# Optimization experiments

Measured on AMD Instinct MI355X. Metric: run time of the kernel, lower is better.

Reference implementation:

```python
import jax, jax.numpy as jnp
import numpy as np

ATOM_FDIM = 39
BOND_FDIM = 11
MAX_NB = 6
N_ATOMS = 100_000
N_BONDS = 200_001  # index 0 is the padding bond
N_MOLS = 1000
HIDDEN = 256
DEPTH = 6


def setup_inputs() -> dict:
    key = jax.random.key(0)
    ks = jax.random.split(key, 8)
    fatoms = jax.random.normal(ks[0], (N_ATOMS, ATOM_FDIM), dtype=jnp.float32)
    fbonds = jax.random.normal(ks[1], (N_BONDS, ATOM_FDIM + BOND_FDIM), dtype=jnp.float32)
    fbonds = fbonds.at[0].set(0.0)  # padding bond has zero features, as in tensorize()
    agraph = jax.random.randint(ks[2], (N_ATOMS, MAX_NB), 0, N_BONDS, dtype=jnp.int64 if jax.config.jax_enable_x64 else jnp.int32)
    bgraph = jax.random.randint(ks[3], (N_BONDS, MAX_NB), 0, N_BONDS, dtype=agraph.dtype)
    bgraph = bgraph.at[0].set(0)
    mol_ids = jnp.sort(jax.random.randint(ks[4], (N_ATOMS,), 0, N_MOLS, dtype=agraph.dtype))
    scale_i = 1.0 / np.sqrt(ATOM_FDIM + BOND_FDIM)
    scale_h = 1.0 / np.sqrt(HIDDEN)
    scale_o = 1.0 / np.sqrt(ATOM_FDIM + HIDDEN)
    W_i = jax.random.normal(ks[5], (HIDDEN, ATOM_FDIM + BOND_FDIM), dtype=jnp.float32) * scale_i
    W_h = jax.random.normal(ks[6], (HIDDEN, HIDDEN), dtype=jnp.float32) * scale_h
    W_o = jax.random.normal(ks[7], (HIDDEN, ATOM_FDIM + HIDDEN), dtype=jnp.float32) * scale_o
    b_o = jnp.zeros((HIDDEN,), dtype=jnp.float32)
    return {
        'fatoms': fatoms, 'fbonds': fbonds, 'agraph': agraph, 'bgraph': bgraph,
        'mol_ids': mol_ids, 'n_mols': N_MOLS, 'depth': DEPTH,
        'W_i': W_i, 'W_h': W_h, 'W_o': W_o, 'b_o': b_o,
    }


def reference(fatoms, fbonds, agraph, bgraph, mol_ids, n_mols, depth, W_i, W_h, W_o, b_o):
    # binput: [E, H]; message passing over directed bond graph
    binput = fbonds @ W_i.T
    message = jax.nn.relu(binput)
    for _ in range(depth - 1):
        nei = message[bgraph].sum(axis=1)          # [E, MAX_NB, H] gather -> [E, H]
        message = jax.nn.relu(binput + nei @ W_h.T)
    nei = message[agraph].sum(axis=1)              # [N, H]
    ainput = jnp.concatenate([fatoms, nei], axis=1)
    atom_hiddens = jax.nn.relu(ainput @ W_o.T + b_o)  # [N, H]
    # per-molecule mean (equivalent to the scope-based slicing mean)
    sums = jax.ops.segment_sum(atom_hiddens, mol_ids, num_segments=n_mols)
    counts = jax.ops.segment_sum(jnp.ones((atom_hiddens.shape[0],), dtype=atom_hiddens.dtype), mol_ids, num_segments=n_mols)
    mol_vecs = sums / jnp.maximum(counts, 1.0)[:, None]
    return mol_vecs
```

## Files before the change

### kernel.cpp

```cpp
#include <hip/hip_runtime.h>

#define HID 256
#define AS_LD 72
#define TB_LD 264

typedef unsigned short u16;
typedef unsigned int u32;
typedef short bf16x8 __attribute__((ext_vector_type(8)));
typedef float f32x4 __attribute__((ext_vector_type(4)));
typedef u16 u16x8 __attribute__((ext_vector_type(8)));

static __device__ __forceinline__ float bf2f(u16 b) {
    u32 u = ((u32)b) << 16;
    return __uint_as_float(u);
}
static __device__ __forceinline__ u16 f2bf(float f) {
    u32 u = __float_as_uint(f);
    return (u16)((u + 0x7FFFu + ((u >> 16) & 1u)) >> 16);
}

__global__ __launch_bounds__(512, 4) void fused_layer(
    const u16* __restrict__ Sg, const int* __restrict__ graph, int c1,
    const u16* __restrict__ Bd, int ldbd, int c2,
    const float* __restrict__ Cf, int ldcf, int Kc, int c3,
    const u16* __restrict__ WB, int ldw,
    const float* __restrict__ bias,
    u16* __restrict__ C, int M)
{
    __shared__ __align__(16) u16 lds[2 * 64 * AS_LD];

    const int t    = threadIdx.x;
    const int w    = t >> 6;
    const int lane = t & 63;
    const int row0 = blockIdx.x * 64;
    const int wc   = w * 32;
    const int fr   = lane & 15;
    const int fq   = lane >> 4;

    const int g  = t & 7;
    const int ra = t >> 3;
    const int gr = row0 + ra;
    const int grc = gr < M ? gr : 0;

    int nbi[6];
    const u16* bdp = nullptr;
    if (c1 > 0) {
        const int* gp = graph + (size_t)grc * 6;
        #pragma unroll
        for (int j = 0; j < 6; ++j) nbi[j] = gp[j];
    }
    if (c2 > 0) bdp = Bd + (size_t)grc * ldbd;

    const int nch = c1 + c2 + c3;
    const int nbf = c1 + c2;

    u16x8 va[6];
    float fa[8];

    auto issue = [&](int kc) {
        if (kc < c1) {
            #pragma unroll
            for (int j = 0; j < 6; ++j)
                va[j] = *(const u16x8*)(Sg + (size_t)nbi[j] * 256 + kc * 64 + g * 8);
        } else if (kc < nbf) {
            va[0] = *(const u16x8*)(bdp + (kc - c1) * 64 + g * 8);
        } else {
            const int kb = (kc - nbf) * 64 + g * 8;
            #pragma unroll
            for (int i = 0; i < 8; ++i)
                fa[i] = (gr < M && kb + i < Kc) ? Cf[(size_t)gr * ldcf + kb + i] : 0.f;
        }
    };

    auto consume = [&](int kc, u16* Ab) {
        u16 o[8];
        if (kc < c1) {
            float sa[8] = {};
            #pragma unroll
            for (int j = 0; j < 6; ++j)
                #pragma unroll
                for (int e = 0; e < 8; ++e) sa[e] += bf2f(va[j][e]);
            #pragma unroll
            for (int e = 0; e < 8; ++e) o[e] = f2bf(sa[e]);
        } else if (kc < nbf) {
            *(u16x8*)o = va[0];
        } else {
            #pragma unroll
            for (int i = 0; i < 8; ++i) o[i] = f2bf(fa[i]);
        }
        *(uint4*)(Ab + ra * AS_LD + g * 8) = *(const uint4*)o;
    };

    f32x4 acc[4][2] = {};
    issue(0);
    #pragma unroll 1
    for (int kc = 0; kc < nch; ++kc) {
        u16* Ab = lds + (kc & 1) * (64 * AS_LD);

        bf16x8 bq[2][2];
        #pragma unroll
        for (int s = 0; s < 2; ++s)
            #pragma unroll
            for (int j = 0; j < 2; ++j) {
                const int col = wc + j * 16 + fr;
                bq[s][j] = *(const bf16x8*)(WB + (size_t)col * ldw + kc * 64 + s * 32 + fq * 8);
            }

        consume(kc, Ab);

        if (kc + 1 < nch) issue(kc + 1);

        asm volatile("s_waitcnt lgkmcnt(0)" ::: "memory");
        __builtin_amdgcn_s_barrier();
        asm volatile("" ::: "memory");

        #pragma unroll
        for (int s = 0; s < 2; ++s) {
            bf16x8 af[4];
            #pragma unroll
            for (int i = 0; i < 4; ++i)
                af[i] = *(const bf16x8*)(Ab + (i * 16 + fr) * AS_LD + s * 32 + fq * 8);
            #pragma unroll
            for (int j = 0; j < 2; ++j)
                #pragma unroll
                for (int i = 0; i < 4; ++i)
                    acc[i][j] = __builtin_amdgcn_mfma_f32_16x16x32_bf16(bq[s][j], af[i], acc[i][j], 0, 0, 0);
        }
    }

    u16* Tb = lds;
    #pragma unroll
    for (int s2 = 0; s2 < 2; ++s2) {
        __syncthreads();
        #pragma unroll
        for (int j = 0; j < 2; ++j) {
            const int gc = wc + j * 16 + fq * 4;
            float4 bv = make_float4(0.f, 0.f, 0.f, 0.f);
            if (bias) bv = *(const float4*)&bias[gc];
            #pragma unroll
            for (int ii = 0; ii < 2; ++ii) {
                const int i = s2 * 2 + ii;
                u16 o[4];
                o[0] = f2bf(fmaxf(acc[i][j][0] + bv.x, 0.f));
                o[1] = f2bf(fmaxf(acc[i][j][1] + bv.y, 0.f));
                o[2] = f2bf(fmaxf(acc[i][j][2] + bv.z, 0.f));
                o[3] = f2bf(fmaxf(acc[i][j][3] + bv.w, 0.f));
                *(uint2*)(Tb + (ii * 16 + fr) * TB_LD + gc) = *(const uint2*)o;
            }
        }
        __syncthreads();
        const int gsl = t & 31;
        const int rb  = t >> 5;
        #pragma unroll
        for (int it2 = 0; it2 < 2; ++it2) {
            const int rl = it2 * 16 + rb;
            const int grr = row0 + s2 * 32 + rl;
            if (grr < M) {
                const u16x8 v = *(const u16x8*)(Tb + rl * TB_LD + gsl * 8);
                *(u16x8*)(C + (size_t)grr * 256 + gsl * 8) = v;
            }
        }
    }
}

__global__ void build_wb(const float* __restrict__ src1, int lds1, int off1, int k1,
                         const float* __restrict__ src2, int lds2, int off2, int k2,
                         u16* __restrict__ dst, int ldd)
{
    const int n = blockIdx.x;
    for (int k = threadIdx.x; k < ldd; k += blockDim.x) {
        float v = 0.f;
        if (k < k1)           v = src1[(size_t)n * lds1 + off1 + k];
        else if (k < k1 + k2) v = src2[(size_t)n * lds2 + off2 + (k - k1)];
        dst[(size_t)n * ldd + k] = f2bf(v);
    }
}

__global__ void build_fb(const float* __restrict__ fb, u16* __restrict__ FB, int E)
{
    const int e = blockIdx.x * 4 + (threadIdx.x >> 6);
    if (e >= E) return;
    const int k = threadIdx.x & 63;
    FB[(size_t)e * 64 + k] = (k < 50) ? f2bf(fb[(size_t)e * 50 + k]) : (u16)0;
}

__global__ void segment_mean(const u16* __restrict__ atomh, const int* __restrict__ mol_ids,
                             float* __restrict__ out, int N)
{
    const int m = blockIdx.x;
    const int t = threadIdx.x;
    __shared__ int s_lo, s_hi;
    if (t == 0) {
        int lo = 0, hi = N;
        while (lo < hi) { int mid = (lo + hi) >> 1; if (mol_ids[mid] < m) lo = mid + 1; else hi = mid; }
        s_lo = lo;
        lo = s_lo; hi = N;
        while (lo < hi) { int mid = (lo + hi) >> 1; if (mol_ids[mid] < m + 1) lo = mid + 1; else hi = mid; }
        s_hi = lo;
    }
    __syncthreads();
    const int lo = s_lo, hi = s_hi;
    float sum = 0.f;
    for (int a = lo; a < hi; ++a) sum += bf2f(atomh[(size_t)a * HID + t]);
    const float cnt = (float)((hi - lo) > 1 ? (hi - lo) : 1);
    out[(size_t)m * HID + t] = sum / cnt;
}

extern "C" void kernel_launch(void* const* d_in, const int* in_sizes, int n_in,
                              void* d_out, int out_size, void* d_ws, size_t ws_size,
                              hipStream_t stream)
{
    const float* fatoms = (const float*)d_in[0];
    const float* fbonds = (const float*)d_in[1];
    const int*   agraph = (const int*)d_in[2];
    const int*   bgraph = (const int*)d_in[3];
    const int*   mol_ids = (const int*)d_in[4];
    const float* W_i = (const float*)d_in[7];
    const float* W_h = (const float*)d_in[8];
    const float* W_o = (const float*)d_in[9];
    const float* b_o = (const float*)d_in[10];

    const int N = in_sizes[0] / 39;
    const int E = in_sizes[1] / 50;
    const int N_MOLS = 1000;
    const int DEPTH = 6;

    const size_t EH = (size_t)E * HID;
    const size_t wbh_sz = (size_t)256 * 320;
    const size_t wbi_sz = (size_t)256 * 64;
    const size_t wbo_sz = (size_t)256 * 320;
    const size_t wsz = wbh_sz + wbi_sz + wbo_sz;
    const size_t fb_sz = (size_t)E * 64;

    const size_t need_nofb = (2 * EH + wsz) * sizeof(u16);
    const size_t need_fb   = (2 * EH + fb_sz + wsz) * sizeof(u16);
    if (ws_size < need_nofb) return;
    const bool use_fb = (ws_size >= need_fb);

    u16* buf0 = (u16*)d_ws;
    u16* buf1 = buf0 + EH;
    u16* FB   = use_fb ? (buf1 + EH) : nullptr;
    u16* wbh  = (use_fb ? FB + fb_sz : buf1 + EH);
    u16* wbi  = wbh + wbh_sz;
    u16* wbo  = wbi + wbi_sz;

    float* out = (float*)d_out;

    build_wb<<<dim3(256), dim3(64), 0, stream>>>(W_h, 256, 0, 256, W_i, 50, 0, 50, wbh, 320);
    build_wb<<<dim3(256), dim3(64), 0, stream>>>(W_i, 50, 0, 50, W_i, 50, 0, 0, wbi, 64);
    build_wb<<<dim3(256), dim3(64), 0, stream>>>(W_o, 295, 39, 256, W_o, 295, 0, 39, wbo, 320);
    if (use_fb)
        build_fb<<<dim3((E + 3) / 4), dim3(256), 0, stream>>>(fbonds, FB, E);

    const int gE = (E + 63) / 64;
    const int gN = (N + 63) / 64;

    if (use_fb)
        fused_layer<<<dim3(gE), dim3(512), 0, stream>>>(
            nullptr, nullptr, 0, FB, 64, 1, nullptr, 0, 0, 0, wbi, 64, nullptr, buf0, E);
    else
        fused_layer<<<dim3(gE), dim3(512), 0, stream>>>(
            nullptr, nullptr, 0, nullptr, 0, 0, fbonds, 50, 50, 1, wbi, 64, nullptr, buf0, E);

    u16* src = buf0;
    u16* dst = buf1;
    for (int it = 0; it < DEPTH - 1; ++it) {
        if (use_fb)
            fused_layer<<<dim3(gE), dim3(512), 0, stream>>>(
                src, bgraph, 4, FB, 64, 1, nullptr, 0, 0, 0, wbh, 320, nullptr, dst, E);
        else
            fused_layer<<<dim3(gE), dim3(512), 0, stream>>>(
                src, bgraph, 4, nullptr, 0, 0, fbonds, 50, 50, 1, wbh, 320, nullptr, dst, E);
        u16* tmp = src; src = dst; dst = tmp;
    }

    fused_layer<<<dim3(gN), dim3(512), 0, stream>>>(
        src, agraph, 4, nullptr, 0, 0, fatoms, 39, 39, 1, wbo, 320, b_o, dst, N);

    segment_mean<<<dim3(N_MOLS), dim3(256), 0, stream>>>(dst, mol_ids, out, N);
}
```

Measured before the change: 914.4 us.

## Store bond messages as uint8 with per-64-column float scales

Message buffers between layers are now written as unsigned 8-bit values with one float scale per 64-column chunk, computed from a wave-shuffle max in the epilogue. The gather stage dequantizes neighbor rows on load, halving the bytes fetched in the memory-bound neighbor-sum. This adds extra scale loads and quantization arithmetic, and loses accuracy relative to bf16 storage, which may break tolerance. The fallback path without the bond-feature buffer is removed and a separate atom-hidden buffer is allocated.

```diff
diff --git a/kernel.cpp b/kernel.cpp
--- a/kernel.cpp
+++ b/kernel.cpp
@@ -5,10 +5,12 @@
 #define TB_LD 264
 
 typedef unsigned short u16;
+typedef unsigned char u8;
 typedef unsigned int u32;
 typedef short bf16x8 __attribute__((ext_vector_type(8)));
 typedef float f32x4 __attribute__((ext_vector_type(4)));
 typedef u16 u16x8 __attribute__((ext_vector_type(8)));
+typedef u8 u8x8 __attribute__((ext_vector_type(8)));
 
 static __device__ __forceinline__ float bf2f(u16 b) {
     u32 u = ((u32)b) << 16;
@@ -20,12 +22,13 @@
 }
 
 __global__ __launch_bounds__(512, 4) void fused_layer(
-    const u16* __restrict__ Sg, const int* __restrict__ graph, int c1,
+    const u8* __restrict__ Sg, const float* __restrict__ Ssc,
+    const int* __restrict__ graph, int c1,
     const u16* __restrict__ Bd, int ldbd, int c2,
     const float* __restrict__ Cf, int ldcf, int Kc, int c3,
     const u16* __restrict__ WB, int ldw,
     const float* __restrict__ bias,
-    u16* __restrict__ C, int M)
+    void* __restrict__ Cout, float* __restrict__ Csc, int M)
 {
     __shared__ __align__(16) u16 lds[2 * 64 * AS_LD];
 
@@ -54,16 +57,21 @@
     const int nch = c1 + c2 + c3;
     const int nbf = c1 + c2;
 
-    u16x8 va[6];
+    u8x8  va[6];
+    float sv[6];
+    u16x8 vb;
     float fa[8];
 
     auto issue = [&](int kc) {
         if (kc < c1) {
             #pragma unroll
             for (int j = 0; j < 6; ++j)
-                va[j] = *(const u16x8*)(Sg + (size_t)nbi[j] * 256 + kc * 64 + g * 8);
+                va[j] = *(const u8x8*)(Sg + (size_t)nbi[j] * 256 + kc * 64 + g * 8);
+            #pragma unroll
+            for (int j = 0; j < 6; ++j)
+                sv[j] = Ssc[(size_t)nbi[j] * 4 + kc];
         } else if (kc < nbf) {
-            va[0] = *(const u16x8*)(bdp + (kc - c1) * 64 + g * 8);
+            vb = *(const u16x8*)(bdp + (kc - c1) * 64 + g * 8);
         } else {
             const int kb = (kc - nbf) * 64 + g * 8;
             #pragma unroll
@@ -79,11 +87,11 @@
             #pragma unroll
             for (int j = 0; j < 6; ++j)
                 #pragma unroll
-                for (int e = 0; e < 8; ++e) sa[e] += bf2f(va[j][e]);
+                for (int e = 0; e < 8; ++e) sa[e] += (float)va[j][e] * sv[j];
             #pragma unroll
             for (int e = 0; e < 8; ++e) o[e] = f2bf(sa[e]);
         } else if (kc < nbf) {
-            *(u16x8*)o = va[0];
+            *(u16x8*)o = vb;
         } else {
             #pragma unroll
             for (int i = 0; i < 8; ++i) o[i] = f2bf(fa[i]);
@@ -129,6 +137,7 @@
     }
 
     u16* Tb = lds;
+    const bool quant = (Csc != nullptr);
     #pragma unroll
     for (int s2 = 0; s2 < 2; ++s2) {
         __syncthreads();
@@ -155,9 +164,27 @@
         for (int it2 = 0; it2 < 2; ++it2) {
             const int rl = it2 * 16 + rb;
             const int grr = row0 + s2 * 32 + rl;
-            if (grr < M) {
-                const u16x8 v = *(const u16x8*)(Tb + rl * TB_LD + gsl * 8);
-                *(u16x8*)(C + (size_t)grr * 256 + gsl * 8) = v;
+            const u16x8 v = *(const u16x8*)(Tb + rl * TB_LD + gsl * 8);
+            if (quant) {
+                float f[8];
+                float mx = 0.f;
+                #pragma unroll
+                for (int e = 0; e < 8; ++e) { f[e] = bf2f(v[e]); mx = fmaxf(mx, f[e]); }
+                mx = fmaxf(mx, __shfl_xor(mx, 1));
+                mx = fmaxf(mx, __shfl_xor(mx, 2));
+                mx = fmaxf(mx, __shfl_xor(mx, 4));
+                const float r = mx > 0.f ? 255.f / mx : 0.f;
+                u8x8 q;
+                #pragma unroll
+                for (int e = 0; e < 8; ++e) q[e] = (u8)(f[e] * r + 0.5f);
+                if (grr < M) {
+                    *(u8x8*)((u8*)Cout + (size_t)grr * 256 + gsl * 8) = q;
+                    if ((gsl & 7) == 0)
+                        Csc[(size_t)grr * 4 + (gsl >> 3)] = mx * (1.f / 255.f);
+                }
+            } else {
+                if (grr < M)
+                    *(u16x8*)((u16*)Cout + (size_t)grr * 256 + gsl * 8) = v;
             }
         }
     }
@@ -225,57 +252,54 @@
     const int N_MOLS = 1000;
     const int DEPTH = 6;
 
-    const size_t EH = (size_t)E * HID;
-    const size_t wbh_sz = (size_t)256 * 320;
-    const size_t wbi_sz = (size_t)256 * 64;
-    const size_t wbo_sz = (size_t)256 * 320;
-    const size_t wsz = wbh_sz + wbi_sz + wbo_sz;
-    const size_t fb_sz = (size_t)E * 64;
-
-    const size_t need_nofb = (2 * EH + wsz) * sizeof(u16);
-    const size_t need_fb   = (2 * EH + fb_sz + wsz) * sizeof(u16);
-    if (ws_size < need_nofb) return;
-    const bool use_fb = (ws_size >= need_fb);
-
-    u16* buf0 = (u16*)d_ws;
-    u16* buf1 = buf0 + EH;
-    u16* FB   = use_fb ? (buf1 + EH) : nullptr;
-    u16* wbh  = (use_fb ? FB + fb_sz : buf1 + EH);
-    u16* wbi  = wbh + wbh_sz;
-    u16* wbo  = wbi + wbi_sz;
+    const size_t q_sz  = (size_t)E * 256;
+    const size_t sc_sz = (size_t)E * 4 * 4;
+    const size_t fb_sz = (size_t)E * 64 * 2;
+    const size_t ah_sz = (size_t)N * HID * 2;
+    const size_t wbh_sz = (size_t)256 * 320 * 2;
+    const size_t wbi_sz = (size_t)256 * 64 * 2;
+    const size_t wbo_sz = (size_t)256 * 320 * 2;
+    const size_t need = 2 * q_sz + 2 * sc_sz + fb_sz + ah_sz + wbh_sz + wbi_sz + wbo_sz;
+    if (ws_size < need) return;
+
+    u8* p = (u8*)d_ws;
+    u8*    q0  = p;             p += q_sz;
+    u8*    q1  = p;             p += q_sz;
+    float* sc0 = (float*)p;     p += sc_sz;
+    float* sc1 = (float*)p;     p += sc_sz;
+    u16*   FB  = (u16*)p;       p += fb_sz;
+    u16*   ah  = (u16*)p;       p += ah_sz;
+    u16*   wbh = (u16*)p;       p += wbh_sz;
+    u16*   wbi = (u16*)p;       p += wbi_sz;
+    u16*   wbo = (u16*)p;
 
     float* out = (float*)d_out;
 
     build_wb<<<dim3(256), dim3(64), 0, stream>>>(W_h, 256, 0, 256, W_i, 50, 0, 50, wbh, 320);
     build_wb<<<dim3(256), dim3(64), 0, stream>>>(W_i, 50, 0, 50, W_i, 50, 0, 0, wbi, 64);
     build_wb<<<dim3(256), dim3(64), 0, stream>>>(W_o, 295, 39, 256, W_o, 295, 0, 39, wbo, 320);
-    if (use_fb)
-        build_fb<<<dim3((E + 3) / 4), dim3(256), 0, stream>>>(fbonds, FB, E);
+    build_fb<<<dim3((E + 3) / 4), dim3(256), 0, stream>>>(fbonds, FB, E);
 
     const int gE = (E + 63) / 64;
     const int gN = (N + 63) / 64;
 
-    if (use_fb)
+    fused_layer<<<dim3(gE), dim3(512), 0, stream>>>(
+        nullptr, nullptr, nullptr, 0, FB, 64, 1, nullptr, 0, 0, 0,
+        wbi, 64, nullptr, q0, sc0, E);
+
+    u8* src = q0;  float* ssc = sc0;
+    u8* dst = q1;  float* dsc = sc1;
+    for (int it = 0; it < DEPTH - 1; ++it) {
         fused_layer<<<dim3(gE), dim3(512), 0, stream>>>(
-            nullptr, nullptr, 0, FB, 64, 1, nullptr, 0, 0, 0, wbi, 64, nullptr, buf0, E);
-    else
-        fused_layer<<<dim3(gE), dim3(512), 0, stream>>>(
-            nullptr, nullptr, 0, nullptr, 0, 0, fbonds, 50, 50, 1, wbi, 64, nullptr, buf0, E);
-
-    u16* src = buf0;
-    u16* dst = buf1;
-    for (int it = 0; it < DEPTH - 1; ++it) {
-        if (use_fb)
-            fused_layer<<<dim3(gE), dim3(512), 0, stream>>>(
-                src, bgraph, 4, FB, 64, 1, nullptr, 0, 0, 0, wbh, 320, nullptr, dst, E);
-        else
-            fused_layer<<<dim3(gE), dim3(512), 0, stream>>>(
-                src, bgraph, 4, nullptr, 0, 0, fbonds, 50, 50, 1, wbh, 320, nullptr, dst, E);
-        u16* tmp = src; src = dst; dst = tmp;
+            src, ssc, bgraph, 4, FB, 64, 1, nullptr, 0, 0, 0,
+            wbh, 320, nullptr, dst, dsc, E);
+        u8* tq = src; src = dst; dst = tq;
+        float* ts = ssc; ssc = dsc; dsc = ts;
     }
 
     fused_layer<<<dim3(gN), dim3(512), 0, stream>>>(
-        src, agraph, 4, nullptr, 0, 0, fatoms, 39, 39, 1, wbo, 320, b_o, dst, N);
-
-    segment_mean<<<dim3(N_MOLS), dim3(256), 0, stream>>>(dst, mol_ids, out, N);
-}
+        src, ssc, agraph, 4, nullptr, 0, 0, fatoms, 39, 39, 1,
+        wbo, 320, b_o, ah, nullptr, N);
+
+    segment_mean<<<dim3(N_MOLS), dim3(256), 0, stream>>>(ah, mol_ids, out, N);
+}
```

New measurement: 3.053 ms. +233.9%, slower.

## Fuse per-molecule segment sum into final atom layer via atomics

Applied to the files above, without the earlier changes.

The final atom-hidden layer no longer writes atom hidden states to global memory. Each block instead sums its rows per molecule in the epilogue and atomically adds the partial sums into the zeroed output. A light normalize kernel then divides by the atom counts. This removes the atomh write and the serial per-molecule read loop, at the cost of float atomics (non-deterministic summation order) and an extra memset.

```diff
diff --git a/kernel.cpp b/kernel.cpp
--- a/kernel.cpp
+++ b/kernel.cpp
@@ -25,9 +25,11 @@
     const float* __restrict__ Cf, int ldcf, int Kc, int c3,
     const u16* __restrict__ WB, int ldw,
     const float* __restrict__ bias,
-    u16* __restrict__ C, int M)
+    u16* __restrict__ C, int M,
+    const int* __restrict__ amol, float* __restrict__ Msum)
 {
     __shared__ __align__(16) u16 lds[2 * 64 * AS_LD];
+    __shared__ int smol[64];
 
     const int t    = threadIdx.x;
     const int w    = t >> 6;
@@ -41,6 +43,9 @@
     const int ra = t >> 3;
     const int gr = row0 + ra;
     const int grc = gr < M ? gr : 0;
+
+    if (Msum != nullptr && t < 64)
+        smol[t] = (row0 + t < M) ? amol[row0 + t] : -1;
 
     int nbi[6];
     const u16* bdp = nullptr;
@@ -149,16 +154,35 @@
             }
         }
         __syncthreads();
-        const int gsl = t & 31;
-        const int rb  = t >> 5;
-        #pragma unroll
-        for (int it2 = 0; it2 < 2; ++it2) {
-            const int rl = it2 * 16 + rb;
-            const int grr = row0 + s2 * 32 + rl;
-            if (grr < M) {
-                const u16x8 v = *(const u16x8*)(Tb + rl * TB_LD + gsl * 8);
-                *(u16x8*)(C + (size_t)grr * 256 + gsl * 8) = v;
+        if (Msum == nullptr) {
+            const int gsl = t & 31;
+            const int rb  = t >> 5;
+            #pragma unroll
+            for (int it2 = 0; it2 < 2; ++it2) {
+                const int rl = it2 * 16 + rb;
+                const int grr = row0 + s2 * 32 + rl;
+                if (grr < M) {
+                    const u16x8 v = *(const u16x8*)(Tb + rl * TB_LD + gsl * 8);
+                    *(u16x8*)(C + (size_t)grr * 256 + gsl * 8) = v;
+                }
             }
+        } else {
+            const int col = t & 255;
+            const int h   = t >> 8;
+            float s = 0.f;
+            int cur = -1;
+            #pragma unroll 1
+            for (int r = h * 16; r < h * 16 + 16; ++r) {
+                const int m = smol[s2 * 32 + r];
+                if (m != cur) {
+                    if (cur >= 0 && s != 0.f)
+                        atomicAdd(&Msum[(size_t)cur * HID + col], s);
+                    cur = m; s = 0.f;
+                }
+                if (m >= 0) s += bf2f(Tb[r * TB_LD + col]);
+            }
+            if (cur >= 0 && s != 0.f)
+                atomicAdd(&Msum[(size_t)cur * HID + col], s);
         }
     }
 }
@@ -184,8 +208,7 @@
     FB[(size_t)e * 64 + k] = (k < 50) ? f2bf(fb[(size_t)e * 50 + k]) : (u16)0;
 }
 
-__global__ void segment_mean(const u16* __restrict__ atomh, const int* __restrict__ mol_ids,
-                             float* __restrict__ out, int N)
+__global__ void normalize_out(const int* __restrict__ mol_ids, float* __restrict__ out, int N)
 {
     const int m = blockIdx.x;
     const int t = threadIdx.x;
@@ -199,11 +222,8 @@
         s_hi = lo;
     }
     __syncthreads();
-    const int lo = s_lo, hi = s_hi;
-    float sum = 0.f;
-    for (int a = lo; a < hi; ++a) sum += bf2f(atomh[(size_t)a * HID + t]);
-    const float cnt = (float)((hi - lo) > 1 ? (hi - lo) : 1);
-    out[(size_t)m * HID + t] = sum / cnt;
+    const int cnt = (s_hi - s_lo) > 1 ? (s_hi - s_lo) : 1;
+    out[(size_t)m * HID + t] *= (1.f / (float)cnt);
 }
 
 extern "C" void kernel_launch(void* const* d_in, const int* in_sizes, int n_in,
@@ -246,6 +266,8 @@
 
     float* out = (float*)d_out;
 
+    hipMemsetAsync(out, 0, (size_t)N_MOLS * HID * sizeof(float), stream);
+
     build_wb<<<dim3(256), dim3(64), 0, stream>>>(W_h, 256, 0, 256, W_i, 50, 0, 50, wbh, 320);
     build_wb<<<dim3(256), dim3(64), 0, stream>>>(W_i, 50, 0, 50, W_i, 50, 0, 0, wbi, 64);
     build_wb<<<dim3(256), dim3(64), 0, stream>>>(W_o, 295, 39, 256, W_o, 295, 0, 39, wbo, 320);
@@ -257,25 +279,30 @@
 
     if (use_fb)
         fused_layer<<<dim3(gE), dim3(512), 0, stream>>>(
-            nullptr, nullptr, 0, FB, 64, 1, nullptr, 0, 0, 0, wbi, 64, nullptr, buf0, E);
+            nullptr, nullptr, 0, FB, 64, 1, nullptr, 0, 0, 0, wbi, 64, nullptr,
+            buf0, E, nullptr, nullptr);
     else
         fused_layer<<<dim3(gE), dim3(512), 0, stream>>>(
-            nullptr, nullptr, 0, nullptr, 0, 0, fbonds, 50, 50, 1, wbi, 64, nullptr, buf0, E);
+            nullptr, nullptr, 0, nullptr, 0, 0, fbonds, 50, 50, 1, wbi, 64, nullptr,
+            buf0, E, nullptr, nullptr);
 
     u16* src = buf0;
     u16* dst = buf1;
     for (int it = 0; it < DEPTH - 1; ++it) {
         if (use_fb)
             fused_layer<<<dim3(gE), dim3(512), 0, stream>>>(
-                src, bgraph, 4, FB, 64, 1, nullptr, 0, 0, 0, wbh, 320, nullptr, dst, E);
+                src, bgraph, 4, FB, 64, 1, nullptr, 0, 0, 0, wbh, 320, nullptr,
+                dst, E, nullptr, nullptr);
         else
             fused_layer<<<dim3(gE), dim3(512), 0, stream>>>(
-                src, bgraph, 4, nullptr, 0, 0, fbonds, 50, 50, 1, wbh, 320, nullptr, dst, E);
+                src, bgraph, 4, nullptr, 0, 0, fbonds, 50, 50, 1, wbh, 320, nullptr,
+                dst, E, nullptr, nullptr);
         u16* tmp = src; src = dst; dst = tmp;
     }
 
     fused_layer<<<dim3(gN), dim3(512), 0, stream>>>(
-        src, agraph, 4, nullptr, 0, 0, fatoms, 39, 39, 1, wbo, 320, b_o, dst, N);
-
-    segment_mean<<<dim3(N_MOLS), dim3(256), 0, stream>>>(dst, mol_ids, out, N);
-}
+        src, agraph, 4, nullptr, 0, 0, fatoms, 39, 39, 1, wbo, 320, b_o,
+        nullptr, N, mol_ids, out);
+
+    normalize_out<<<dim3(N_MOLS), dim3(256), 0, stream>>>(mol_ids, out, N);
+}
```

Measured after the change: 871.4 us. -4.7%, faster.
